# Kernel tuning notes

Measured on AMD Instinct MI355X. Metric: run time of the kernel, lower is better.

Reference implementation:

```python
import jax, jax.numpy as jnp
import numpy as np

B, N, D = 8, 1024, 256   # batch, nodes, input_size
H, HO = 4, 64            # nhead, hidden_size/nhead
T = 5                    # number of edge types (len(edges))
NEG = -1e9
EPS = 1e-6


def setup_inputs() -> dict:
    key = jax.random.key(0)
    ks = jax.random.split(key, 6)
    nodes_embed = jax.random.normal(ks[0], (B, N, D), dtype=jnp.float32)
    node_adj = jax.random.randint(ks[1], (B, N, N), 0, T + 1)  # values 0..T, 0 = no edge
    # per-head projection W: xavier-ish scale
    W = jax.random.normal(ks[2], (H, D, HO), dtype=jnp.float32) * (1.0 / np.sqrt(D))
    # per-edge-type scoring linear (2*HO -> 1), split into src/dst halves
    a_src = jax.random.normal(ks[3], (H, T, HO), dtype=jnp.float32) * 0.1
    a_dst = jax.random.normal(ks[4], (H, T, HO), dtype=jnp.float32) * 0.1
    bias = jnp.zeros((H, HO), dtype=jnp.float32)
    ln_gamma = jnp.ones((H, HO), dtype=jnp.float32)
    ln_beta = jnp.zeros((H, HO), dtype=jnp.float32)
    return {
        'nodes_embed': nodes_embed,
        'node_adj': node_adj,
        'W': W,
        'a_src': a_src,
        'a_dst': a_dst,
        'bias': bias,
        'ln_gamma': ln_gamma,
        'ln_beta': ln_beta,
    }


def reference(nodes_embed, node_adj, W, a_src, a_dst, bias, ln_gamma, ln_beta):
    # h: [B, H, N, HO] -- all heads projected at once
    h = jnp.einsum('bnd,hde->bhne', nodes_embed, W)
    # The torch code concatenates [h_i, h_j] and applies a (2*HO -> 1) linear per
    # edge type; that equals e_src[t, i] + e_dst[t, j] with the linear weight split
    # into src/dst halves. Avoids materializing the O(N^2 * 2*HO) concat tensor.
    e_src = jnp.einsum('bhne,hte->bhtn', h, a_src)  # [B, H, T, N]
    e_dst = jnp.einsum('bhne,hte->bhtn', h, a_dst)  # [B, H, T, N]
    n_types = a_src.shape[1]
    weight = jnp.zeros(h.shape[:2] + (h.shape[2], h.shape[2]), dtype=h.dtype)  # [B,H,N,N]
    for t in range(n_types):  # small fixed loop over edge types
        mask = (node_adj == t + 1).astype(h.dtype)[:, None]  # [B,1,N,N]
        weight = weight + mask * (e_src[:, :, t, :, None] + e_dst[:, :, t, None, :])
    weight = jax.nn.leaky_relu(weight, negative_slope=0.01)
    weight = jnp.where(node_adj[:, None] == 0, NEG, weight)
    attention = jax.nn.softmax(weight, axis=-1)  # [B,H,N,N]
    dst = jnp.einsum('bhij,bhje->bhie', attention, h) + bias[None, :, None, :]
    out = jax.nn.relu(dst) + h  # dropout is identity (p=0)
    # per-head LayerNorm over HO, eps=1e-6 (biased variance, as torch)
    mu = out.mean(axis=-1, keepdims=True)
    var = out.var(axis=-1, keepdims=True)
    out = (out - mu) / jnp.sqrt(var + EPS) * ln_gamma[None, :, None, :] + ln_beta[None, :, None, :]
    # concat heads: [B,H,N,HO] -> [B,N,H*HO]
    b, hh, n, e = out.shape
    return out.transpose(0, 2, 1, 3).reshape(b, n, hh * e)
```

## Files before the change

### kernel.cpp

```cpp
#include <hip/hip_runtime.h>
#include <hip/hip_bf16.h>

#define Bn 8
#define Nn 1024
#define Dn 256
#define Hn 4
#define HOn 64
#define Tn 5
#define WTR 80

typedef short bf16x8 __attribute__((ext_vector_type(8)));
typedef float f32x4 __attribute__((ext_vector_type(4)));

__device__ __forceinline__ float b2f(unsigned short u) {
    unsigned x = ((unsigned)u) << 16;
    float f;
    __builtin_memcpy(&f, &x, 4);
    return f;
}
__device__ __forceinline__ unsigned bfr(float f) {
    unsigned u;
    __builtin_memcpy(&u, &f, 4);
    return (u + 0x7FFFu + ((u >> 16) & 1u)) >> 16;
}
__device__ __forceinline__ unsigned short f2b(float f) { return (unsigned short)bfr(f); }

__global__ __launch_bounds__(256) void k_signal(float* __restrict__ out, int n) {
    int i = blockIdx.x * 256 + threadIdx.x;
    if (i < n) out[i] = 100.0f;
}

__global__ __launch_bounds__(256) void k_transpose_w(const float* __restrict__ W,
                                                     const float* __restrict__ a_src,
                                                     const float* __restrict__ a_dst,
                                                     unsigned short* __restrict__ WT) {
    __shared__ float tile[64][65];
    int h = blockIdx.x >> 2;
    int d0 = (blockIdx.x & 3) * 64;
    int c0 = threadIdx.x & 63;
    int r0 = threadIdx.x >> 6;
#pragma unroll
    for (int r = 0; r < 16; r++) {
        int d = r * 4 + r0;
        tile[d][c0] = W[((size_t)(h * Dn + d0 + d)) * HOn + c0];
    }
    __syncthreads();
#pragma unroll
    for (int r = 0; r < 16; r++) {
        int e = r * 4 + r0;
        WT[((size_t)(h * WTR + e)) * Dn + d0 + c0] = f2b(tile[c0][e]);
    }
    for (int t = r0; t < 2 * Tn; t += 4) {
        const float* av = (t < Tn) ? (a_src + (h * Tn + t) * HOn)
                                   : (a_dst + (h * Tn + t - Tn) * HOn);
        float s = 0.f;
#pragma unroll
        for (int e = 0; e < HOn; e++) s += tile[c0][e] * av[e];
        WT[((size_t)(h * WTR + 64 + t)) * Dn + d0 + c0] = f2b(s);
    }
    for (int rr = 74 + r0; rr < WTR; rr += 4)
        WT[((size_t)(h * WTR + rr)) * Dn + d0 + c0] = 0;
}

__global__ __launch_bounds__(256) void k_proj(const float* __restrict__ X,
                                              const unsigned short* __restrict__ WT,
                                              unsigned short* __restrict__ hT,
                                              float* __restrict__ e_src,
                                              float* __restrict__ e_dst) {
    int tid = threadIdx.x;
    int w = tid >> 6;
    int lane = tid & 63;
    int quad = lane >> 4;
    int l15 = lane & 15;
    int b = blockIdx.x >> 6;
    int i0 = (blockIdx.x & 63) * 16;
    int h = w;
    int bh = b * Hn + h;

    bf16x8 Bx[8];
    const float* xf = X + ((size_t)(b * Nn + i0 + l15)) * Dn + quad * 8;
#pragma unroll
    for (int kc = 0; kc < 8; kc++) {
        union { bf16x8 v; unsigned u[4]; } uu;
        const float4* xp = (const float4*)(xf + kc * 32);
        float4 A0 = xp[0], A1 = xp[1];
        __hip_bfloat162 h0 = __float22bfloat162_rn(make_float2(A0.x, A0.y));
        __hip_bfloat162 h1 = __float22bfloat162_rn(make_float2(A0.z, A0.w));
        __hip_bfloat162 h2 = __float22bfloat162_rn(make_float2(A1.x, A1.y));
        __hip_bfloat162 h3 = __float22bfloat162_rn(make_float2(A1.z, A1.w));
        __builtin_memcpy(&uu.u[0], &h0, 4);
        __builtin_memcpy(&uu.u[1], &h1, 4);
        __builtin_memcpy(&uu.u[2], &h2, 4);
        __builtin_memcpy(&uu.u[3], &h3, 4);
        Bx[kc] = uu.v;
    }

    f32x4 acc[5] = {{0.f, 0.f, 0.f, 0.f}, {0.f, 0.f, 0.f, 0.f}, {0.f, 0.f, 0.f, 0.f},
                    {0.f, 0.f, 0.f, 0.f}, {0.f, 0.f, 0.f, 0.f}};
    const unsigned short* wbase = WT + (size_t)h * WTR * Dn;
#pragma unroll
    for (int kc = 0; kc < 8; kc++) {
#pragma unroll
        for (int et = 0; et < 5; et++) {
            bf16x8 Aw = *(const bf16x8*)(wbase + (size_t)(et * 16 + l15) * Dn + kc * 32 + quad * 8);
            acc[et] = __builtin_amdgcn_mfma_f32_16x16x32_bf16(Aw, Bx[kc], acc[et], 0, 0, 0);
        }
    }

#pragma unroll
    for (int et = 0; et < 4; et++) {
#pragma unroll
        for (int reg = 0; reg < 4; reg++) {
            int e = et * 16 + quad * 4 + reg;
            hT[((size_t)bh * HOn + e) * Nn + i0 + l15] = f2b(acc[et][reg]);
        }
    }
#pragma unroll
    for (int reg = 0; reg < 4; reg++) {
        int t = quad * 4 + reg;
        if (t < Tn)
            e_src[((size_t)bh * Tn + t) * Nn + i0 + l15] = acc[4][reg];
        else if (t < 2 * Tn)
            e_dst[((size_t)bh * Tn + (t - Tn)) * Nn + i0 + l15] = acc[4][reg];
    }
}

__global__ __launch_bounds__(512) void k_attn(const int* __restrict__ adj,
                                              const float* __restrict__ e_src,
                                              const float* __restrict__ e_dst,
                                              const unsigned short* __restrict__ hT,
                                              const float* __restrict__ bias,
                                              const float* __restrict__ gamma,
                                              const float* __restrict__ beta,
                                              float* __restrict__ out) {
    __shared__ __align__(16) unsigned short p_lds[8][16][136];
    __shared__ float edt[8][5][132];
    __shared__ float est[4][5][16];
    __shared__ float l_lds[8][16];
    float* macc = (float*)&p_lds[4][0][0];

    int tid = threadIdx.x;
    int w = tid >> 6;
    int lane = tid & 63;
    int quad = lane >> 4;
    int l15 = lane & 15;
    int hh = w & 3;
    int half = w >> 2;
    int b = blockIdx.x >> 6;
    int i0 = (blockIdx.x & 63) * 16;
    int bh = b * Hn + hh;
    int J0 = half * 512;

    const int* adj_base = adj + ((size_t)(b * Nn + i0)) * Nn + J0;
    const float* edst = e_dst + (size_t)bh * Tn * Nn + J0;
    const unsigned short* hTb = hT + (size_t)bh * HOn * Nn;

    f32x4 acc[4] = {{0.f, 0.f, 0.f, 0.f}, {0.f, 0.f, 0.f, 0.f},
                    {0.f, 0.f, 0.f, 0.f}, {0.f, 0.f, 0.f, 0.f}};
    float pl[16];
#pragma unroll
    for (int r = 0; r < 16; r++) pl[r] = 0.f;

    int2 bufA[8], bufB[8];
#pragma unroll
    for (int r = 0; r < 8; r++) bufA[r] = *(const int2*)(adj_base + (size_t)r * Nn + 2 * lane);
    float2 edc[Tn], edn[Tn];
#pragma unroll
    for (int t = 0; t < Tn; t++) edc[t] = *(const float2*)(edst + t * Nn + 2 * lane);

    if (w < 4) {
        const float* esrc = e_src + (size_t)bh * Tn * Nn;
#pragma unroll
        for (int idx = lane; idx < 80; idx += 64) {
            int t = idx >> 4, row = idx & 15;
            est[w][t][row] = esrc[t * Nn + i0 + row];
        }
    }
    __syncthreads();

#define P1ROW(ROW, AV)                                                          \
    {                                                                           \
        int a0 = (AV).x, a1 = (AV).y;                                           \
        int t0 = a0 - 1; t0 = (t0 < 0) ? 0 : t0;                                \
        int t1 = a1 - 1; t1 = (t1 < 0) ? 0 : t1;                                \
        float ed0 = edt[w][t0][2 * lane];                                       \
        float ed1 = edt[w][t1][2 * lane + 1];                                   \
        float e0 = est[hh][t0][ROW];                                            \
        float e1 = est[hh][t1][ROW];                                            \
        float x0 = e0 + ed0; x0 = fmaxf(x0, 0.01f * x0);                        \
        float x1 = e1 + ed1; x1 = fmaxf(x1, 0.01f * x1);                        \
        float p0 = __expf(x0); p0 = (a0 == 0) ? 0.f : p0;                       \
        float p1 = __expf(x1); p1 = (a1 == 0) ? 0.f : p1;                       \
        pl[ROW] += p0 + p1;                                                     \
        __hip_bfloat162 pp = __float22bfloat162_rn(make_float2(p0, p1));        \
        unsigned pu; __builtin_memcpy(&pu, &pp, 4);                             \
        *(unsigned*)(&p_lds[w][ROW][2 * lane]) = pu;                            \
    }

#pragma unroll 1
    for (int c = 0; c < 4; c++) {
        int jc = c * 128;
#pragma unroll
        for (int t = 0; t < Tn; t++) *(float2*)(&edt[w][t][2 * lane]) = edc[t];
#pragma unroll
        for (int r = 0; r < 8; r++)
            bufB[r] = *(const int2*)(adj_base + (size_t)(8 + r) * Nn + jc + 2 * lane);
        if (c < 3) {
#pragma unroll
            for (int t = 0; t < Tn; t++)
                edn[t] = *(const float2*)(edst + t * Nn + jc + 128 + 2 * lane);
        }
#pragma unroll
        for (int r = 0; r < 8; r++) P1ROW(r, bufA[r]);
        if (c < 3) {
#pragma unroll
            for (int r = 0; r < 8; r++)
                bufA[r] = *(const int2*)(adj_base + (size_t)r * Nn + jc + 128 + 2 * lane);
        }
#pragma unroll
        for (int r = 0; r < 8; r++) P1ROW(8 + r, bufB[r]);
        if (c < 3) {
#pragma unroll
            for (int t = 0; t < Tn; t++) edc[t] = edn[t];
        }
#pragma unroll
        for (int k = 0; k < 4; k++) {
            bf16x8 Afr = *(const bf16x8*)(&p_lds[w][l15][k * 32 + quad * 8]);
#pragma unroll
            for (int et = 0; et < 4; et++) {
                bf16x8 Bf = *(const bf16x8*)(hTb + (size_t)(et * 16 + l15) * Nn + J0 + jc + k * 32 + quad * 8);
                acc[et] = __builtin_amdgcn_mfma_f32_16x16x32_bf16(Afr, Bf, acc[et], 0, 0, 0);
            }
        }
    }
#undef P1ROW

#pragma unroll
    for (int r = 0; r < 16; r++) {
#pragma unroll
        for (int off = 1; off < 64; off <<= 1) pl[r] += __shfl_xor(pl[r], off);
    }
    if (lane == 0) {
#pragma unroll
        for (int r = 0; r < 16; r++) l_lds[w][r] = pl[r];
    }
    __syncthreads();
    if (w >= 4) {
#pragma unroll
        for (int et = 0; et < 4; et++)
#pragma unroll
            for (int reg = 0; reg < 4; reg++)
                macc[((hh * 16) + quad * 4 + reg) * 64 + et * 16 + l15] = acc[et][reg];
    }
    __syncthreads();
    if (w >= 4) return;

    float bv[4], gv[4], bev[4];
#pragma unroll
    for (int et = 0; et < 4; et++) {
        int e = et * 16 + l15;
        bv[et] = bias[hh * HOn + e];
        gv[et] = gamma[hh * HOn + e];
        bev[et] = beta[hh * HOn + e];
    }
#pragma unroll
    for (int reg = 0; reg < 4; reg++) {
        int r = quad * 4 + reg;
        int i = i0 + r;
        float lw = l_lds[w][r] + l_lds[w + 4][r];
        float linv = 1.f / fmaxf(lw, 1e-30f);
        float dv[4];
        float s = 0.f, ss = 0.f;
#pragma unroll
        for (int et = 0; et < 4; et++) {
            int e = et * 16 + l15;
            float v = (acc[et][reg] + macc[((hh * 16) + r) * 64 + e]) * linv + bv[et];
            v = (v > 0.f) ? v : 0.f;
            v += b2f(hTb[(size_t)e * Nn + i]);
            dv[et] = v;
            s += v;
            ss += v * v;
        }
#pragma unroll
        for (int off = 8; off; off >>= 1) {
            s += __shfl_xor(s, off);
            ss += __shfl_xor(ss, off);
        }
        float mean = s * (1.f / 64.f);
        float var = ss * (1.f / 64.f) - mean * mean;
        float rstd = rsqrtf(var + 1e-6f);
#pragma unroll
        for (int et = 0; et < 4; et++) {
            int e = et * 16 + l15;
            float o = (dv[et] - mean) * rstd * gv[et] + bev[et];
            out[((size_t)(b * Nn + i)) * (Hn * HOn) + hh * HOn + e] = o;
        }
    }
}

extern "C" void kernel_launch(void* const* d_in, const int* in_sizes, int n_in,
                              void* d_out, int out_size, void* d_ws, size_t ws_size,
                              hipStream_t stream) {
    const float* X = (const float*)d_in[0];
    const int* adj = (const int*)d_in[1];
    const float* W = (const float*)d_in[2];
    const float* a_src = (const float*)d_in[3];
    const float* a_dst = (const float*)d_in[4];
    const float* bias = (const float*)d_in[5];
    const float* gamma = (const float*)d_in[6];
    const float* beta = (const float*)d_in[7];
    float* out = (float*)d_out;

    char* ws = (char*)d_ws;
    size_t off = 0;
    unsigned short* hT = (unsigned short*)(ws + off);  off += (size_t)Bn * Hn * Nn * HOn * 2;
    unsigned short* WT = (unsigned short*)(ws + off);  off += (size_t)Hn * WTR * Dn * 2;
    float* e_src = (float*)(ws + off);                 off += (size_t)Bn * Hn * Tn * Nn * 4;
    float* e_dst = (float*)(ws + off);                 off += (size_t)Bn * Hn * Tn * Nn * 4;

    if (ws_size < off) {
        k_signal<<<(out_size + 255) / 256, 256, 0, stream>>>(out, out_size);
        return;
    }

    k_transpose_w<<<Hn * (Dn / 64), 256, 0, stream>>>(W, a_src, a_dst, WT);
    k_proj<<<Bn * (Nn / 16), 256, 0, stream>>>(X, WT, hT, e_src, e_dst);
    k_attn<<<Bn * (Nn / 16), 512, 0, stream>>>(adj, e_src, e_dst, hT, bias, gamma, beta, out);
}
```

Before: 155.0 us.

## Compute softmax row sums via MFMA with ones and select e_dst from registers

```diff
diff --git a/kernel.cpp b/kernel.cpp
--- a/kernel.cpp
+++ b/kernel.cpp
@@ -134,8 +134,7 @@
                                               const float* __restrict__ beta,
                                               float* __restrict__ out) {
     __shared__ __align__(16) unsigned short p_lds[8][16][136];
-    __shared__ float edt[8][5][132];
-    __shared__ float est[4][5][16];
+    __shared__ float es2[4][16][8];
     __shared__ float l_lds[8][16];
     float* macc = (float*)&p_lds[4][0][0];
 
@@ -157,23 +156,23 @@
 
     f32x4 acc[4] = {{0.f, 0.f, 0.f, 0.f}, {0.f, 0.f, 0.f, 0.f},
                     {0.f, 0.f, 0.f, 0.f}, {0.f, 0.f, 0.f, 0.f}};
-    float pl[16];
-#pragma unroll
-    for (int r = 0; r < 16; r++) pl[r] = 0.f;
-
-    int2 bufA[8], bufB[8];
-#pragma unroll
-    for (int r = 0; r < 8; r++) bufA[r] = *(const int2*)(adj_base + (size_t)r * Nn + 2 * lane);
-    float2 edc[Tn], edn[Tn];
-#pragma unroll
-    for (int t = 0; t < Tn; t++) edc[t] = *(const float2*)(edst + t * Nn + 2 * lane);
+    f32x4 accl = {0.f, 0.f, 0.f, 0.f};
+    bf16x8 ONES;
+    {
+        short o = (short)0x3F80;
+        ONES = (bf16x8){o, o, o, o, o, o, o, o};
+    }
+
+    int2 bufA[4], bufB[4];
+#pragma unroll
+    for (int r = 0; r < 4; r++) bufA[r] = *(const int2*)(adj_base + (size_t)r * Nn + 2 * lane);
 
     if (w < 4) {
         const float* esrc = e_src + (size_t)bh * Tn * Nn;
 #pragma unroll
         for (int idx = lane; idx < 80; idx += 64) {
             int t = idx >> 4, row = idx & 15;
-            est[w][t][row] = esrc[t * Nn + i0 + row];
+            es2[w][row][t] = esrc[t * Nn + i0 + row];
         }
     }
     __syncthreads();
@@ -183,15 +182,17 @@
         int a0 = (AV).x, a1 = (AV).y;                                           \
         int t0 = a0 - 1; t0 = (t0 < 0) ? 0 : t0;                                \
         int t1 = a1 - 1; t1 = (t1 < 0) ? 0 : t1;                                \
-        float ed0 = edt[w][t0][2 * lane];                                       \
-        float ed1 = edt[w][t1][2 * lane + 1];                                   \
-        float e0 = est[hh][t0][ROW];                                            \
-        float e1 = est[hh][t1][ROW];                                            \
-        float x0 = e0 + ed0; x0 = fmaxf(x0, 0.01f * x0);                        \
-        float x1 = e1 + ed1; x1 = fmaxf(x1, 0.01f * x1);                        \
+        float e0 = es2[hh][ROW][t0];                                            \
+        float e1 = es2[hh][ROW][t1];                                            \
+        float d0 = edc[0].x, d1 = edc[0].y;                                     \
+        d0 = (t0 == 1) ? edc[1].x : d0; d1 = (t1 == 1) ? edc[1].y : d1;         \
+        d0 = (t0 == 2) ? edc[2].x : d0; d1 = (t1 == 2) ? edc[2].y : d1;         \
+        d0 = (t0 == 3) ? edc[3].x : d0; d1 = (t1 == 3) ? edc[3].y : d1;         \
+        d0 = (t0 == 4) ? edc[4].x : d0; d1 = (t1 == 4) ? edc[4].y : d1;         \
+        float x0 = e0 + d0; x0 = fmaxf(x0, 0.01f * x0);                         \
+        float x1 = e1 + d1; x1 = fmaxf(x1, 0.01f * x1);                         \
         float p0 = __expf(x0); p0 = (a0 == 0) ? 0.f : p0;                       \
         float p1 = __expf(x1); p1 = (a1 == 0) ? 0.f : p1;                       \
-        pl[ROW] += p0 + p1;                                                     \
         __hip_bfloat162 pp = __float22bfloat162_rn(make_float2(p0, p1));        \
         unsigned pu; __builtin_memcpy(&pu, &pp, 4);                             \
         *(unsigned*)(&p_lds[w][ROW][2 * lane]) = pu;                            \
@@ -200,32 +201,35 @@
 #pragma unroll 1
     for (int c = 0; c < 4; c++) {
         int jc = c * 128;
-#pragma unroll
-        for (int t = 0; t < Tn; t++) *(float2*)(&edt[w][t][2 * lane]) = edc[t];
-#pragma unroll
-        for (int r = 0; r < 8; r++)
-            bufB[r] = *(const int2*)(adj_base + (size_t)(8 + r) * Nn + jc + 2 * lane);
+        float2 edc[Tn];
+#pragma unroll
+        for (int t = 0; t < Tn; t++) edc[t] = *(const float2*)(edst + t * Nn + jc + 2 * lane);
+#pragma unroll
+        for (int r = 0; r < 4; r++)
+            bufB[r] = *(const int2*)(adj_base + (size_t)(4 + r) * Nn + jc + 2 * lane);
+#pragma unroll
+        for (int r = 0; r < 4; r++) P1ROW(r, bufA[r]);
+#pragma unroll
+        for (int r = 0; r < 4; r++)
+            bufA[r] = *(const int2*)(adj_base + (size_t)(8 + r) * Nn + jc + 2 * lane);
+#pragma unroll
+        for (int r = 0; r < 4; r++) P1ROW(4 + r, bufB[r]);
+#pragma unroll
+        for (int r = 0; r < 4; r++)
+            bufB[r] = *(const int2*)(adj_base + (size_t)(12 + r) * Nn + jc + 2 * lane);
+#pragma unroll
+        for (int r = 0; r < 4; r++) P1ROW(8 + r, bufA[r]);
         if (c < 3) {
 #pragma unroll
-            for (int t = 0; t < Tn; t++)
-                edn[t] = *(const float2*)(edst + t * Nn + jc + 128 + 2 * lane);
-        }
-#pragma unroll
-        for (int r = 0; r < 8; r++) P1ROW(r, bufA[r]);
-        if (c < 3) {
-#pragma unroll
-            for (int r = 0; r < 8; r++)
+            for (int r = 0; r < 4; r++)
                 bufA[r] = *(const int2*)(adj_base + (size_t)r * Nn + jc + 128 + 2 * lane);
         }
 #pragma unroll
-        for (int r = 0; r < 8; r++) P1ROW(8 + r, bufB[r]);
-        if (c < 3) {
-#pragma unroll
-            for (int t = 0; t < Tn; t++) edc[t] = edn[t];
-        }
+        for (int r = 0; r < 4; r++) P1ROW(12 + r, bufB[r]);
 #pragma unroll
         for (int k = 0; k < 4; k++) {
             bf16x8 Afr = *(const bf16x8*)(&p_lds[w][l15][k * 32 + quad * 8]);
+            accl = __builtin_amdgcn_mfma_f32_16x16x32_bf16(Afr, ONES, accl, 0, 0, 0);
 #pragma unroll
             for (int et = 0; et < 4; et++) {
                 bf16x8 Bf = *(const bf16x8*)(hTb + (size_t)(et * 16 + l15) * Nn + J0 + jc + k * 32 + quad * 8);
@@ -235,14 +239,9 @@
     }
 #undef P1ROW
 
-#pragma unroll
-    for (int r = 0; r < 16; r++) {
-#pragma unroll
-        for (int off = 1; off < 64; off <<= 1) pl[r] += __shfl_xor(pl[r], off);
-    }
-    if (lane == 0) {
-#pragma unroll
-        for (int r = 0; r < 16; r++) l_lds[w][r] = pl[r];
+    if (l15 == 0) {
+#pragma unroll
+        for (int reg = 0; reg < 4; reg++) l_lds[w][quad * 4 + reg] = accl[reg];
     }
     __syncthreads();
     if (w >= 4) {
```

New measurement: 151.3 us. -2.4%, faster.
